# Performance work log

Hardware: AMD Instinct MI355X
Metric: run time of the kernel (lower is better)

## Reference

```python
import jax, jax.numpy as jnp
import numpy as np

DIM = 256
HEADS = 8
DIM_HEAD = 64
INNER = HEADS * DIM_HEAD  # 512
SCALE = DIM_HEAD ** -0.5
B, H, W = 8, 64, 64


def setup_inputs() -> dict:
    key = jax.random.key(0)
    ks = jax.random.split(key, 6)
    x = jax.random.normal(ks[0], (B, DIM, H, W), dtype=jnp.float32)
    W_proj = jax.random.normal(ks[1], (DIM, INNER), dtype=jnp.float32) * (DIM ** -0.5)
    step_rep = jax.random.normal(ks[2], (HEADS, 1, 1), dtype=jnp.float32)
    step_x = jax.random.normal(ks[3], (HEADS, 1, 1), dtype=jnp.float32)
    W_out = jax.random.normal(ks[4], (INNER, DIM), dtype=jnp.float32) * (INNER ** -0.5)
    b_out = jax.random.normal(ks[5], (DIM,), dtype=jnp.float32) * 0.01
    return {"x": x, "W_proj": W_proj, "step_rep": step_rep, "step_x": step_x,
            "W_out": W_out, "b_out": b_out}


def _attention(q, k, v):
    # q: [b,h,m,d], k/v: [b,h,n,d]
    dots = jnp.einsum('bhmd,bhnd->bhmn', q, k) * SCALE
    attn = jax.nn.softmax(dots, axis=-1)
    out = jnp.einsum('bhmn,bhnd->bhmd', attn, v)
    return out, attn


def reference(x, W_proj, step_rep, step_x, W_out, b_out):
    b, c, h, w = x.shape
    n = h * w
    # b c h w -> b (h w) c
    x_seq = jnp.transpose(x, (0, 2, 3, 1)).reshape(b, n, c)
    proj = x_seq @ W_proj  # [b, n, inner]
    # AdaptiveAvgPool2d((8,8)) over the (h,w) grid; h,w divisible by 8 -> exact block mean
    proj_2d = proj.reshape(b, h, w, INNER)
    rep = proj_2d.reshape(b, 8, h // 8, 8, w // 8, INNER).mean(axis=(2, 4))  # [b,8,8,inner]
    rep = rep.reshape(b, 64, INNER)
    # split heads
    proj_h = proj.reshape(b, n, HEADS, DIM_HEAD).transpose(0, 2, 1, 3)  # [b,heads,n,dh]
    rep_h = rep.reshape(b, 64, HEADS, DIM_HEAD).transpose(0, 2, 1, 3)   # [b,heads,64,dh]
    # stage 1: 64 pooled queries attend to n keys
    rep_delta, attn = _attention(rep_h, proj_h, proj_h)  # attn: [b,heads,64,n]
    rep2 = rep_h + step_rep * rep_delta
    # stage 2: self-attention among the 64 pooled tokens
    x_delta, _ = _attention(rep2, rep2, rep2)  # [b,heads,64,dh]
    # back-project via attn^T
    x_delta = jnp.einsum('bhmn,bhmd->bhnd', attn, x_delta)  # [b,heads,n,dh]
    x_delta = step_x * x_delta
    # b h n k -> b n (h k)
    x_delta = x_delta.transpose(0, 2, 1, 3).reshape(b, n, INNER)
    x_out = x_delta @ W_out + b_out  # [b, n, dim]
    return x_out.reshape(b, h, w, c).transpose(0, 3, 1, 2)
```

## Files before the change

kernel.cpp:

```cpp
#include <hip/hip_runtime.h>
#include <cstdint>
#include <cstddef>


#define SCALE 0.125f

typedef __attribute__((ext_vector_type(8))) short bf16x8;
typedef __attribute__((ext_vector_type(4))) float f32x4;
typedef __attribute__((ext_vector_type(16))) float f32x16;
typedef __attribute__((ext_vector_type(4))) unsigned int u32x4;

#define MFMA32(a, b, c) __builtin_amdgcn_mfma_f32_32x32x16_bf16(a, b, c, 0, 0, 0)
#define MFMA16(a, b, c) __builtin_amdgcn_mfma_f32_16x16x32_bf16(a, b, c, 0, 0, 0)

__device__ __forceinline__ unsigned short f2bf(float x) {
  unsigned int u = __float_as_uint(x);
  u += 0x7FFFu + ((u >> 16) & 1u);
  return (unsigned short)(u >> 16);
}
__device__ __forceinline__ float bf2f(unsigned short b) {
  return __uint_as_float(((unsigned int)b) << 16);
}
__device__ __forceinline__ void split2(float x, unsigned short& h, unsigned short& l) {
  h = f2bf(x);
  l = f2bf(x - bf2f(h));
}
__device__ __forceinline__ unsigned int cvtpk(float lo, float hi_) {
  unsigned int r;
  asm("v_cvt_pk_bf16_f32 %0, %1, %2" : "=v"(r) : "v"(lo), "v"(hi_));
  return r;
}

typedef const __attribute__((address_space(1))) unsigned int* gas_ptr;
typedef __attribute__((address_space(3))) unsigned int* las_ptr;
__device__ __forceinline__ void gload16(const void* g, void* l) {
  __builtin_amdgcn_global_load_lds((gas_ptr)(size_t)g,
                                   (las_ptr)(unsigned int)(size_t)l, 16, 0, 0);
}

__global__ __launch_bounds__(256) void tsplit(
    const float* __restrict__ in, long long in_bs,
    unsigned short* __restrict__ oh, unsigned short* __restrict__ ol,
    long long o_bs, int R, int C) {
  __shared__ float T[32][33];
  int bz = blockIdx.z;
  const float* ip = in + (size_t)bz * in_bs;
  unsigned short* oph = oh + (size_t)bz * o_bs;
  unsigned short* opl = ol + (size_t)bz * o_bs;
  int c0 = blockIdx.x * 32, r0 = blockIdx.y * 32;
  int t = threadIdx.x;
  int col = t & 31, row8 = t >> 5;
#pragma unroll
  for (int i = 0; i < 4; i++)
    T[row8 + i * 8][col] = ip[(size_t)(r0 + row8 + i * 8) * C + c0 + col];
  __syncthreads();
  int cp = (t & 15) * 2, rr = t >> 4;
#pragma unroll
  for (int i = 0; i < 2; i++) {
    int orow = rr + i * 16;
    float v0 = T[cp][orow], v1 = T[cp + 1][orow];
    unsigned short h0, l0, h1, l1;
    split2(v0, h0, l0);
    split2(v1, h1, l1);
    size_t o = (size_t)(c0 + orow) * R + r0 + cp;
    *(unsigned int*)(oph + o) = (unsigned int)h0 | ((unsigned int)h1 << 16);
    *(unsigned int*)(opl + o) = (unsigned int)l0 | ((unsigned int)l1 << 16);
  }
}

template <int BT>
__global__ __launch_bounds__(256) void gemm_mfma(
    const unsigned short* __restrict__ Ah, const unsigned short* __restrict__ Al,
    long long a_bs,
    const unsigned short* __restrict__ Bh, const unsigned short* __restrict__ Bl,
    long long b_bs,
    float* __restrict__ Cf, unsigned short* __restrict__ Ch,
    unsigned short* __restrict__ Cl, long long c_bs,
    int M, int N, int K, const float* __restrict__ bias, int lnx, int lny) {
  __shared__ unsigned short lds[2][4][128][32];
  int id0 = blockIdx.x;
  int cpx = gridDim.x >> 3;
  int id = (id0 & 7) * cpx + (id0 >> 3);
  int bx = id & ((1 << lnx) - 1);
  int by = (id >> lnx) & ((1 << lny) - 1);
  int bz = id >> (lnx + lny);
  int m0 = by * 128, n0 = bx * 128;
  int tid = threadIdx.x;
  int wave = tid >> 6, lane = tid & 63;
  int wr = wave >> 1, wc = wave & 1;

  const unsigned short* src;
  int r0g, sBeg = 0, nS = 8, dArr = wave;
  if (wave == 0) {
    src = Ah + (size_t)bz * a_bs; r0g = m0;
  } else if (wave == 1) {
    src = Al + (size_t)bz * a_bs; r0g = m0;
  } else if (BT == 2) {
    src = ((wave == 2) ? Bh : Bl) + (size_t)bz * b_bs; r0g = n0;
  } else {
    src = Bh + (size_t)bz * b_bs; r0g = n0; dArr = 2;
    sBeg = (wave - 2) * 4; nS = 4;
  }
  int q = lane >> 2;
  int chunk = (lane & 3) ^ ((q >> 1) & 3);
  const unsigned short* srow = src + (size_t)(r0g + q) * K + chunk * 8;

  int g = lane >> 4, fr = lane & 15;
  int slot = (g ^ ((fr >> 1) & 3)) * 8;
  int offA = (wr * 64 + fr) * 32 + slot;
  int offB = 2 * 4096 + (wc * 64 + fr) * 32 + slot;

  f32x4 acc[4][4];
#pragma unroll
  for (int i = 0; i < 4; i++)
#pragma unroll
    for (int j = 0; j < 4; j++)
#pragma unroll
      for (int r = 0; r < 4; r++) acc[i][j][r] = 0.0f;

  int nt = K >> 5;
  for (int s5 = 0; s5 < nS; ++s5) {
    int ss = sBeg + s5;
    gload16(srow + (size_t)(ss * 16) * K, &lds[0][dArr][ss * 16][0]);
  }
  __syncthreads();
  int cur = 0;
  for (int t0 = 0; t0 < nt; ++t0) {
    if (t0 + 1 < nt) {
      int k0 = (t0 + 1) << 5;
      for (int s5 = 0; s5 < nS; ++s5) {
        int ss = sBeg + s5;
        gload16(srow + (size_t)(ss * 16) * K + k0, &lds[cur ^ 1][dArr][ss * 16][0]);
      }
    }
    const unsigned short* bb = &lds[cur][0][0][0];
    bf16x8 af[2][4], bfv[2][4];
#pragma unroll
    for (int i = 0; i < 4; i++) {
      af[0][i] = *(const bf16x8*)(bb + offA + i * 512);
      af[1][i] = *(const bf16x8*)(bb + 4096 + offA + i * 512);
      bfv[0][i] = *(const bf16x8*)(bb + offB + i * 512);
      if (BT == 2) bfv[1][i] = *(const bf16x8*)(bb + 4096 + offB + i * 512);
    }
#pragma unroll
    for (int i = 0; i < 4; i++)
#pragma unroll
      for (int j = 0; j < 4; j++) {
        acc[i][j] = MFMA16(af[0][i], bfv[0][j], acc[i][j]);
        if (BT == 2) acc[i][j] = MFMA16(af[0][i], bfv[1][j], acc[i][j]);
        acc[i][j] = MFMA16(af[1][i], bfv[0][j], acc[i][j]);
      }
    __syncthreads();
    cur ^= 1;
  }
  int mBase = m0 + wr * 64 + g * 4;
  int nBase = n0 + wc * 64 + fr;
  if (Cf) {
    float* Cb = Cf + (size_t)bz * c_bs;
#pragma unroll
    for (int i = 0; i < 4; i++)
#pragma unroll
      for (int qd = 0; qd < 4; qd++) {
        int m = mBase + i * 16 + qd;
        float bi = bias ? bias[m] : 0.0f;
#pragma unroll
        for (int j = 0; j < 4; j++)
          Cb[(size_t)m * N + nBase + j * 16] = acc[i][j][qd] + bi;
      }
  } else {
    unsigned short* Chb = Ch + (size_t)bz * c_bs;
    unsigned short* Clb = Cl + (size_t)bz * c_bs;
#pragma unroll
    for (int i = 0; i < 4; i++)
#pragma unroll
      for (int qd = 0; qd < 4; qd++) {
        int m = mBase + i * 16 + qd;
#pragma unroll
        for (int j = 0; j < 4; j++) {
          unsigned short hh, ll;
          split2(acc[i][j][qd], hh, ll);
          Chb[(size_t)m * N + nBase + j * 16] = hh;
          Clb[(size_t)m * N + nBase + j * 16] = ll;
        }
      }
  }
}

__global__ __launch_bounds__(256) void tpool(
    const unsigned short* __restrict__ projh, const unsigned short* __restrict__ projl,
    unsigned short* __restrict__ projTh,
    unsigned short* __restrict__ reph, unsigned short* __restrict__ repl) {
  __shared__ unsigned short Lh[64][64];
  __shared__ unsigned short Ll[64][64];
  int it = blockIdx.x, py = blockIdx.y, b = blockIdx.z;
  int t = threadIdx.x;
  int ch = t & 63, seg = t >> 6;
  int swc = ((ch ^ (ch >> 3)) & 7) << 3;
  float poolacc[2] = {0.0f, 0.0f};

  for (int dy = 0; dy < 8; dy++) {
    int base_n = py * 512 + dy * 64;
    {
      int rl = t >> 3, cq = (t & 7) * 8;
#pragma unroll
      for (int p = 0; p < 2; p++) {
        int row = rl + p * 32;
        size_t ga = ((size_t)(b * 4096 + base_n + row)) * 512 + it * 64 + cq;
        bf16x8 vh = *(const bf16x8*)(projh + ga);
        bf16x8 vl = *(const bf16x8*)(projl + ga);
#pragma unroll
        for (int j = 0; j < 8; j++) {
          int cl = cq + j;
          int sw = ((cl ^ (cl >> 3)) & 7) << 3;
          Lh[cl][row ^ sw] = (unsigned short)vh[j];
          Ll[cl][row ^ sw] = (unsigned short)vl[j];
        }
      }
    }
    __syncthreads();
#pragma unroll
    for (int half = 0; half < 2; half++) {
      int n0 = seg * 16 + half * 8;
      int n0x = n0 ^ swc;
      bf16x8 rh = *(const bf16x8*)&Lh[ch][n0x];
      bf16x8 rl8 = *(const bf16x8*)&Ll[ch][n0x];
      size_t o = ((size_t)(b * 512 + it * 64 + ch)) * 4096 + base_n + n0;
      *(bf16x8*)(projTh + o) = rh;
      float ssum = 0.0f;
#pragma unroll
      for (int j = 0; j < 8; j++)
        ssum += bf2f((unsigned short)rh[j]) + bf2f((unsigned short)rl8[j]);
      poolacc[half] += ssum;
    }
    __syncthreads();
  }
#pragma unroll
  for (int half = 0; half < 2; half++) {
    float v = poolacc[half] * 0.015625f;
    unsigned short hh, ll;
    split2(v, hh, ll);
    size_t ro = ((size_t)(b * 64 + py * 8 + seg * 2 + half)) * 512 + it * 64 + ch;
    reph[ro] = hh;
    repl[ro] = ll;
  }
}

__global__ __launch_bounds__(256) void fattn(
    const unsigned short* __restrict__ projh,
    const unsigned short* __restrict__ reph, const unsigned short* __restrict__ repl,
    const unsigned short* __restrict__ projTh,
    unsigned short* __restrict__ PTh,
    float* __restrict__ pvpart, float* __restrict__ lpart) {
  int bh = blockIdx.x, s = blockIdx.y;
  int b = bh >> 3, h = bh & 7;
  int t = threadIdx.x;
  int wave = t >> 6, lane = t & 63;
  int lm = lane & 31, hi = lane >> 5;

  bf16x8 qf[2][4][2];
#pragma unroll
  for (int mt = 0; mt < 2; mt++)
#pragma unroll
    for (int ks = 0; ks < 4; ks++) {
      size_t qo = ((size_t)(b * 64 + mt * 32 + lm)) * 512 + h * 64 + ks * 16 + hi * 8;
      qf[mt][ks][0] = *(const bf16x8*)(reph + qo);
      qf[mt][ks][1] = *(const bf16x8*)(repl + qo);
    }

  f32x16 pv[2][2];
#pragma unroll
  for (int a = 0; a < 2; a++)
#pragma unroll
    for (int c = 0; c < 2; c++)
#pragma unroll
      for (int r = 0; r < 16; r++) pv[a][c][r] = 0.0f;
  float lsum0 = 0.0f, lsum1 = 0.0f;

  for (int sti = 0; sti < 2; sti++) {
    int n0 = s * 512 + (wave * 2 + sti) * 64;
#pragma unroll
    for (int nn = 0; nn < 64; nn += 32) {
      int nb = n0 + nn;
      f32x16 sa0, sa1;
#pragma unroll
      for (int r = 0; r < 16; r++) { sa0[r] = 0.0f; sa1[r] = 0.0f; }
      __builtin_amdgcn_s_setprio(1);
#pragma unroll
      for (int ks = 0; ks < 4; ks++) {
        size_t ko = ((size_t)(b * 4096 + nb + lm)) * 512 + h * 64 + ks * 16 + hi * 8;
        bf16x8 kh = *(const bf16x8*)(projh + ko);
        sa0 = MFMA32(kh, qf[0][ks][0], sa0);
        sa0 = MFMA32(kh, qf[0][ks][1], sa0);
        sa1 = MFMA32(kh, qf[1][ks][0], sa1);
        sa1 = MFMA32(kh, qf[1][ks][1], sa1);
      }
      __builtin_amdgcn_s_setprio(0);
#pragma unroll
      for (int r = 0; r < 16; r++) {
        sa0[r] = __expf(sa0[r] * SCALE); lsum0 += sa0[r];
        sa1[r] = __expf(sa1[r] * SCALE); lsum1 += sa1[r];
      }
      {
        int kk0 = h * 64 + lm, kk1 = kk0 + 32;
#pragma unroll
        for (int r = 0; r < 16; r++) {
          int n = nb + (r & 3) + 8 * (r >> 2) + 4 * hi;
          size_t o = ((size_t)(b * 4096 + n)) * 512;
          PTh[o + kk0] = f2bf(sa0[r]);
          PTh[o + kk1] = f2bf(sa1[r]);
        }
      }
#pragma unroll
      for (int kc = 0; kc < 2; kc++) {
        bf16x8 paH[2], paL[2];
#pragma unroll
        for (int mt = 0; mt < 2; mt++) {
          float pq[8], lq[8];
#pragma unroll
          for (int qi = 0; qi < 8; qi++) {
            float v = (mt == 0) ? sa0[kc * 8 + qi] : sa1[kc * 8 + qi];
            unsigned short ph_ = f2bf(v);
            pq[qi] = v;
            lq[qi] = v - bf2f(ph_);
          }
          int c01 = (int)cvtpk(pq[0], pq[1]), c23 = (int)cvtpk(pq[2], pq[3]);
          int c45 = (int)cvtpk(pq[4], pq[5]), c67 = (int)cvtpk(pq[6], pq[7]);
          int d01 = __shfl_xor(c01, 32), d23 = __shfl_xor(c23, 32);
          int d45 = __shfl_xor(c45, 32), d67 = __shfl_xor(c67, 32);
          u32x4 wv;
          wv.x = (unsigned int)(hi ? d45 : c01);
          wv.y = (unsigned int)(hi ? d67 : c23);
          wv.z = (unsigned int)(hi ? c45 : d01);
          wv.w = (unsigned int)(hi ? c67 : d23);
          paH[mt] = __builtin_bit_cast(bf16x8, wv);
          int e01 = (int)cvtpk(lq[0], lq[1]), e23 = (int)cvtpk(lq[2], lq[3]);
          int e45 = (int)cvtpk(lq[4], lq[5]), e67 = (int)cvtpk(lq[6], lq[7]);
          int f01 = __shfl_xor(e01, 32), f23 = __shfl_xor(e23, 32);
          int f45 = __shfl_xor(e45, 32), f67 = __shfl_xor(e67, 32);
          u32x4 lv;
          lv.x = (unsigned int)(hi ? f45 : e01);
          lv.y = (unsigned int)(hi ? f67 : e23);
          lv.z = (unsigned int)(hi ? e45 : f01);
          lv.w = (unsigned int)(hi ? e67 : f23);
          paL[mt] = __builtin_bit_cast(bf16x8, lv);
        }
#pragma unroll
        for (int dt = 0; dt < 2; dt++) {
          size_t vto = ((size_t)(b * 512 + h * 64 + dt * 32 + lm)) * 4096 +
                       nb + kc * 16 + hi * 8;
          bf16x8 vh = *(const bf16x8*)(projTh + vto);
          __builtin_amdgcn_s_setprio(1);
          pv[0][dt] = MFMA32(paH[0], vh, pv[0][dt]);
          pv[0][dt] = MFMA32(paL[0], vh, pv[0][dt]);
          pv[1][dt] = MFMA32(paH[1], vh, pv[1][dt]);
          pv[1][dt] = MFMA32(paL[1], vh, pv[1][dt]);
          __builtin_amdgcn_s_setprio(0);
        }
      }
    }
  }
  lsum0 += __shfl_xor(lsum0, 32);
  lsum1 += __shfl_xor(lsum1, 32);
  __shared__ float pvbuf[64][64];
  __shared__ float lbuf[4][64];
  if (hi == 0) { lbuf[wave][lm] = lsum0; lbuf[wave][32 + lm] = lsum1; }
  for (int w = 0; w < 4; w++) {
    __syncthreads();
    if (wave == w) {
#pragma unroll
      for (int mt = 0; mt < 2; mt++)
#pragma unroll
        for (int dt = 0; dt < 2; dt++)
#pragma unroll
          for (int r = 0; r < 16; r++) {
            int m = mt * 32 + (r & 3) + 8 * (r >> 2) + 4 * hi;
            int d = dt * 32 + lm;
            if (w == 0) pvbuf[m][d] = pv[mt][dt][r];
            else pvbuf[m][d] += pv[mt][dt][r];
          }
    }
  }
  __syncthreads();
  size_t base = ((size_t)(s * 64 + bh)) * 4096;
  for (int idx = t; idx < 4096; idx += 256)
    pvpart[base + idx] = pvbuf[idx >> 6][idx & 63];
  if (t < 64)
    lpart[((size_t)(s * 64 + bh)) * 64 + t] =
        lbuf[0][t] + lbuf[1][t] + lbuf[2][t] + lbuf[3][t];
}

__global__ __launch_bounds__(256) void merge_k(
    const float* __restrict__ pvpart, const float* __restrict__ lpart,
    const unsigned short* __restrict__ reph, const unsigned short* __restrict__ repl,
    const float* __restrict__ step_rep, float* __restrict__ rep2,
    float* __restrict__ linv) {
  int bh = blockIdx.x, qy = blockIdx.y;
  int b = bh >> 3, h = bh & 7;
  float sr = step_rep[h];
  int t = threadIdx.x;
  __shared__ float lt[64];
  if (t < 64) {
    float L = 0.0f;
#pragma unroll
    for (int ss = 0; ss < 8; ss++) L += lpart[((size_t)(ss * 64 + bh)) * 64 + t];
    float inv = 1.0f / L;
    lt[t] = inv;
    if (qy == 0) linv[bh * 64 + t] = inv;
  }
  __syncthreads();
#pragma unroll
  for (int k2 = 0; k2 < 4; k2++) {
    int idx = qy * 1024 + k2 * 256 + t;
    int m = idx >> 6, d = idx & 63;
    float sum = 0.0f;
#pragma unroll
    for (int ss = 0; ss < 8; ss++)
      sum += pvpart[((size_t)(ss * 64 + bh)) * 4096 + idx];
    size_t ro = ((size_t)(b * 64 + m)) * 512 + h * 64 + d;
    float repv = bf2f(reph[ro]) + bf2f(repl[ro]);
    rep2[(size_t)bh * 4096 + idx] = repv + sr * sum * lt[m];
  }
}

__global__ __launch_bounds__(256) void stage2_k(
    const float* __restrict__ rep2, const float* __restrict__ Wo,
    const float* __restrict__ step_x, const float* __restrict__ linv,
    unsigned short* __restrict__ GTh, unsigned short* __restrict__ GTl) {
  __shared__ float T[64][68];
  __shared__ float P[64][68];
  __shared__ float Wl[64][68];
  int bh = blockIdx.x, h = bh & 7, b = bh >> 3;
  int t = threadIdx.x;
  int mi = t >> 2, dq = (t & 3) * 16;
#pragma unroll
  for (int j = 0; j < 4; j++) {
    float4 v = *(const float4*)(rep2 + ((size_t)bh * 64 + mi) * 64 + dq + j * 4);
    T[dq + j * 4 + 0][mi] = v.x; T[dq + j * 4 + 1][mi] = v.y;
    T[dq + j * 4 + 2][mi] = v.z; T[dq + j * 4 + 3][mi] = v.w;
  }
  __syncthreads();
  int tx = t & 15, ty = t >> 4;
  {
    float acc[4][4] = {};
#pragma unroll
    for (int k = 0; k < 64; k++) {
      float4 a = *(const float4*)&T[k][ty * 4];
      float4 bv = *(const float4*)&T[k][tx * 4];
      float aa[4] = {a.x, a.y, a.z, a.w};
      float bb[4] = {bv.x, bv.y, bv.z, bv.w};
#pragma unroll
      for (int i = 0; i < 4; i++)
#pragma unroll
        for (int j = 0; j < 4; j++) acc[i][j] += aa[i] * bb[j];
    }
#pragma unroll
    for (int i = 0; i < 4; i++)
      *(float4*)&P[ty * 4 + i][tx * 4] =
          make_float4(acc[i][0] * SCALE, acc[i][1] * SCALE, acc[i][2] * SCALE,
                      acc[i][3] * SCALE);
  }
  __syncthreads();
  if (t < 64) {
    float mx = -3.4e38f;
    for (int n = 0; n < 64; n++) mx = fmaxf(mx, P[t][n]);
    float s = 0.0f;
    for (int n = 0; n < 64; n++) {
      float e = __expf(P[t][n] - mx);
      P[t][n] = e;
      s += e;
    }
    float r = 1.0f / s;
    for (int n = 0; n < 64; n++) P[t][n] *= r;
  }
  __syncthreads();
  float xacc[4][4] = {};
#pragma unroll
  for (int k = 0; k < 64; k++) {
    float aa[4], bb[4];
#pragma unroll
    for (int i = 0; i < 4; i++) {
      aa[i] = P[ty * 4 + i][k];
      bb[i] = T[tx * 4 + i][k];
    }
#pragma unroll
    for (int i = 0; i < 4; i++)
#pragma unroll
      for (int j = 0; j < 4; j++) xacc[i][j] += aa[i] * bb[j];
  }
  __syncthreads();
#pragma unroll
  for (int i = 0; i < 4; i++)
    *(float4*)&P[ty * 4 + i][tx * 4] =
        make_float4(xacc[i][0], xacc[i][1], xacc[i][2], xacc[i][3]);
  float sxh = step_x[h];
  float li[4];
#pragma unroll
  for (int i = 0; i < 4; i++) li[i] = linv[bh * 64 + ty * 4 + i] * sxh;
  int wk = t >> 2, wcq = (t & 3) * 16;
  for (int cb = 0; cb < 4; cb++) {
    __syncthreads();
#pragma unroll
    for (int j = 0; j < 4; j++)
      *(float4*)&Wl[wk][wcq + j * 4] =
          *(const float4*)(Wo + ((size_t)(h * 64 + wk)) * 256 + cb * 64 + wcq + j * 4);
    __syncthreads();
    float gacc[4][4] = {};
#pragma unroll
    for (int k = 0; k < 64; k++) {
      float aa[4];
#pragma unroll
      for (int i = 0; i < 4; i++) aa[i] = P[ty * 4 + i][k];
      float4 bv = *(const float4*)&Wl[k][tx * 4];
      float bb[4] = {bv.x, bv.y, bv.z, bv.w};
#pragma unroll
      for (int i = 0; i < 4; i++)
#pragma unroll
        for (int j = 0; j < 4; j++) gacc[i][j] += aa[i] * bb[j];
    }
#pragma unroll
    for (int i = 0; i < 4; i++)
#pragma unroll
      for (int j = 0; j < 4; j++) {
        float val = gacc[i][j] * li[i];
        size_t o = ((size_t)(b * 256 + cb * 64 + tx * 4 + j)) * 512 + h * 64 + ty * 4 + i;
        unsigned short hh, ll;
        split2(val, hh, ll);
        GTh[o] = hh;
        GTl[o] = ll;
      }
  }
}

extern "C" void kernel_launch(void* const* d_in, const int* in_sizes, int n_in,
                              void* d_out, int out_size, void* d_ws, size_t ws_size,
                              hipStream_t stream) {
  const float* x = (const float*)d_in[0];
  const float* Wp = (const float*)d_in[1];
  const float* srep = (const float*)d_in[2];
  const float* sx = (const float*)d_in[3];
  const float* Wo = (const float*)d_in[4];
  const float* bo = (const float*)d_in[5];
  float* out = (float*)d_out;

  char* wsb = (char*)d_ws;
  unsigned short* projh = (unsigned short*)(wsb + 0);
  unsigned short* projl = (unsigned short*)(wsb + 33554432);
  unsigned short* xTh   = (unsigned short*)(wsb + 67108864);
  unsigned short* xTl   = (unsigned short*)(wsb + 83886080);
  unsigned short* projTh= (unsigned short*)(wsb + 67108864);
  unsigned short* WpTh  = (unsigned short*)(wsb + 100663296);
  unsigned short* WpTl  = (unsigned short*)(wsb + 100925440);
  unsigned short* PTh   = (unsigned short*)(wsb + 100663296);
  unsigned short* reph  = (unsigned short*)(wsb + 134217728);
  unsigned short* repl  = (unsigned short*)(wsb + 134742016);
  float*  pvpart        = (float*)(wsb + 135266304);
  float*  lpart         = (float*)(wsb + 143654912);
  float*  rep2          = (float*)(wsb + 0);
  float*  linv          = (float*)(wsb + 1048576);
  unsigned short* GTh   = (unsigned short*)(wsb + 2097152);
  unsigned short* GTl   = (unsigned short*)(wsb + 4194304);

  tsplit<<<dim3(128, 8, 8), 256, 0, stream>>>(x, (long long)256 * 4096,
                                              xTh, xTl, (long long)4096 * 256, 256, 4096);
  tsplit<<<dim3(16, 8, 1), 256, 0, stream>>>(Wp, 0, WpTh, WpTl, 0, 256, 512);
  gemm_mfma<2><<<dim3(1024), 256, 0, stream>>>(
      xTh, xTl, (long long)4096 * 256, WpTh, WpTl, 0,
      nullptr, projh, projl, (long long)4096 * 512, 4096, 512, 256, nullptr,
      2, 5);
  tpool<<<dim3(8, 8, 8), 256, 0, stream>>>(projh, projl, projTh, reph, repl);
  fattn<<<dim3(64, 8), 256, 0, stream>>>(projh, reph, repl, projTh, PTh,
                                         pvpart, lpart);
  merge_k<<<dim3(64, 4), 256, 0, stream>>>(pvpart, lpart, reph, repl, srep,
                                           rep2, linv);
  stage2_k<<<dim3(64), 256, 0, stream>>>(rep2, Wo, sx, linv, GTh, GTl);
  gemm_mfma<1><<<dim3(512), 256, 0, stream>>>(
      GTh, GTl, (long long)256 * 512, PTh, nullptr, (long long)4096 * 512,
      out, nullptr, nullptr, (long long)256 * 4096, 256, 4096, 512, bo,
      5, 1);
}
```

Measured before the change: 236.7 us.

## Drop low-half split of proj, fuse merge into stage2, stage GEMM epilogue via LDS

The projection GEMM now uses one bf16 part of W_proj and writes proj as a single bf16 tensor with no low residual. This cuts one MFMA per tile, the projl writes, and the tpool reads of projl. The GEMM epilogue is staged through LDS so global stores are vectorized, and the merge and stage2 kernels are fused into one launch. The cost is lower precision for proj and the pooled rep, plus a 64-block fused kernel that may underuse the GPU.

After: 231.2 us. 2.3% less time.

```diff
diff --git a/kernel.cpp b/kernel.cpp
--- a/kernel.cpp
+++ b/kernel.cpp
@@ -68,16 +68,14 @@
   }
 }
 
-template <int BT>
-__global__ __launch_bounds__(256) void gemm_mfma(
+template <bool F32OUT>
+__global__ __launch_bounds__(256) void gemm_sb(
     const unsigned short* __restrict__ Ah, const unsigned short* __restrict__ Al,
     long long a_bs,
-    const unsigned short* __restrict__ Bh, const unsigned short* __restrict__ Bl,
-    long long b_bs,
-    float* __restrict__ Cf, unsigned short* __restrict__ Ch,
-    unsigned short* __restrict__ Cl, long long c_bs,
+    const unsigned short* __restrict__ Bh, long long b_bs,
+    float* __restrict__ Cf, unsigned short* __restrict__ Ch, long long c_bs,
     int M, int N, int K, const float* __restrict__ bias, int lnx, int lny) {
-  __shared__ unsigned short lds[2][4][128][32];
+  __shared__ unsigned short lds[2][3][128][32];
   int id0 = blockIdx.x;
   int cpx = gridDim.x >> 3;
   int id = (id0 & 7) * cpx + (id0 >> 3);
@@ -90,17 +88,10 @@
   int wr = wave >> 1, wc = wave & 1;
 
   const unsigned short* src;
-  int r0g, sBeg = 0, nS = 8, dArr = wave;
-  if (wave == 0) {
-    src = Ah + (size_t)bz * a_bs; r0g = m0;
-  } else if (wave == 1) {
-    src = Al + (size_t)bz * a_bs; r0g = m0;
-  } else if (BT == 2) {
-    src = ((wave == 2) ? Bh : Bl) + (size_t)bz * b_bs; r0g = n0;
-  } else {
-    src = Bh + (size_t)bz * b_bs; r0g = n0; dArr = 2;
-    sBeg = (wave - 2) * 4; nS = 4;
-  }
+  int r0g, sBeg, nS, dArr;
+  if (wave == 0) { src = Ah + (size_t)bz * a_bs; r0g = m0; sBeg = 0; nS = 8; dArr = 0; }
+  else if (wave == 1) { src = Al + (size_t)bz * a_bs; r0g = m0; sBeg = 0; nS = 8; dArr = 1; }
+  else { src = Bh + (size_t)bz * b_bs; r0g = n0; sBeg = (wave - 2) * 4; nS = 4; dArr = 2; }
   int q = lane >> 2;
   int chunk = (lane & 3) ^ ((q >> 1) & 3);
   const unsigned short* srow = src + (size_t)(r0g + q) * K + chunk * 8;
@@ -134,64 +125,69 @@
       }
     }
     const unsigned short* bb = &lds[cur][0][0][0];
-    bf16x8 af[2][4], bfv[2][4];
+    bf16x8 af[2][4], bfv[4];
 #pragma unroll
     for (int i = 0; i < 4; i++) {
       af[0][i] = *(const bf16x8*)(bb + offA + i * 512);
       af[1][i] = *(const bf16x8*)(bb + 4096 + offA + i * 512);
-      bfv[0][i] = *(const bf16x8*)(bb + offB + i * 512);
-      if (BT == 2) bfv[1][i] = *(const bf16x8*)(bb + 4096 + offB + i * 512);
+      bfv[i] = *(const bf16x8*)(bb + offB + i * 512);
     }
 #pragma unroll
     for (int i = 0; i < 4; i++)
 #pragma unroll
       for (int j = 0; j < 4; j++) {
-        acc[i][j] = MFMA16(af[0][i], bfv[0][j], acc[i][j]);
-        if (BT == 2) acc[i][j] = MFMA16(af[0][i], bfv[1][j], acc[i][j]);
-        acc[i][j] = MFMA16(af[1][i], bfv[0][j], acc[i][j]);
+        acc[i][j] = MFMA16(af[0][i], bfv[j], acc[i][j]);
+        acc[i][j] = MFMA16(af[1][i], bfv[j], acc[i][j]);
       }
     __syncthreads();
     cur ^= 1;
   }
-  int mBase = m0 + wr * 64 + g * 4;
-  int nBase = n0 + wc * 64 + fr;
-  if (Cf) {
-    float* Cb = Cf + (size_t)bz * c_bs;
-#pragma unroll
-    for (int i = 0; i < 4; i++)
-#pragma unroll
-      for (int qd = 0; qd < 4; qd++) {
-        int m = mBase + i * 16 + qd;
-        float bi = bias ? bias[m] : 0.0f;
-#pragma unroll
-        for (int j = 0; j < 4; j++)
-          Cb[(size_t)m * N + nBase + j * 16] = acc[i][j][qd] + bi;
-      }
-  } else {
-    unsigned short* Chb = Ch + (size_t)bz * c_bs;
-    unsigned short* Clb = Cl + (size_t)bz * c_bs;
-#pragma unroll
-    for (int i = 0; i < 4; i++)
-#pragma unroll
-      for (int qd = 0; qd < 4; qd++) {
-        int m = mBase + i * 16 + qd;
-#pragma unroll
-        for (int j = 0; j < 4; j++) {
-          unsigned short hh, ll;
-          split2(acc[i][j][qd], hh, ll);
-          Chb[(size_t)m * N + nBase + j * 16] = hh;
-          Clb[(size_t)m * N + nBase + j * 16] = ll;
-        }
-      }
+
+  float* eld = (float*)(&lds[0][0][0][0]) + wave * 1088;
+  int rr = lane >> 2, cb = (lane & 3) * 16;
+#pragma unroll
+  for (int i = 0; i < 4; i++) {
+#pragma unroll
+    for (int j = 0; j < 4; j++)
+#pragma unroll
+      for (int qd = 0; qd < 4; qd++)
+        eld[(g * 4 + qd) * 68 + fr + j * 16] = acc[i][j][qd];
+    __syncthreads();
+    int mrow = m0 + wr * 64 + i * 16 + rr;
+    int ncol = n0 + wc * 64 + cb;
+    float4 v0 = *(const float4*)(eld + rr * 68 + cb);
+    float4 v1 = *(const float4*)(eld + rr * 68 + cb + 4);
+    float4 v2 = *(const float4*)(eld + rr * 68 + cb + 8);
+    float4 v3 = *(const float4*)(eld + rr * 68 + cb + 12);
+    if (F32OUT) {
+      float bi = bias ? bias[mrow] : 0.0f;
+      float* Cb = Cf + (size_t)bz * c_bs + (size_t)mrow * N + ncol;
+      *(float4*)(Cb + 0) = make_float4(v0.x + bi, v0.y + bi, v0.z + bi, v0.w + bi);
+      *(float4*)(Cb + 4) = make_float4(v1.x + bi, v1.y + bi, v1.z + bi, v1.w + bi);
+      *(float4*)(Cb + 8) = make_float4(v2.x + bi, v2.y + bi, v2.z + bi, v2.w + bi);
+      *(float4*)(Cb + 12) = make_float4(v3.x + bi, v3.y + bi, v3.z + bi, v3.w + bi);
+    } else {
+      float vv[16] = {v0.x, v0.y, v0.z, v0.w, v1.x, v1.y, v1.z, v1.w,
+                      v2.x, v2.y, v2.z, v2.w, v3.x, v3.y, v3.z, v3.w};
+      bf16x8 p0, p1;
+#pragma unroll
+      for (int k = 0; k < 8; k++) {
+        p0[k] = (short)f2bf(vv[k]);
+        p1[k] = (short)f2bf(vv[8 + k]);
+      }
+      unsigned short* Cb = Ch + (size_t)bz * c_bs + (size_t)mrow * N + ncol;
+      *(bf16x8*)(Cb + 0) = p0;
+      *(bf16x8*)(Cb + 8) = p1;
+    }
+    __syncthreads();
   }
 }
 
 __global__ __launch_bounds__(256) void tpool(
-    const unsigned short* __restrict__ projh, const unsigned short* __restrict__ projl,
+    const unsigned short* __restrict__ projh,
     unsigned short* __restrict__ projTh,
     unsigned short* __restrict__ reph, unsigned short* __restrict__ repl) {
   __shared__ unsigned short Lh[64][64];
-  __shared__ unsigned short Ll[64][64];
   int it = blockIdx.x, py = blockIdx.y, b = blockIdx.z;
   int t = threadIdx.x;
   int ch = t & 63, seg = t >> 6;
@@ -207,13 +203,11 @@
         int row = rl + p * 32;
         size_t ga = ((size_t)(b * 4096 + base_n + row)) * 512 + it * 64 + cq;
         bf16x8 vh = *(const bf16x8*)(projh + ga);
-        bf16x8 vl = *(const bf16x8*)(projl + ga);
 #pragma unroll
         for (int j = 0; j < 8; j++) {
           int cl = cq + j;
           int sw = ((cl ^ (cl >> 3)) & 7) << 3;
           Lh[cl][row ^ sw] = (unsigned short)vh[j];
-          Ll[cl][row ^ sw] = (unsigned short)vl[j];
         }
       }
     }
@@ -223,13 +217,11 @@
       int n0 = seg * 16 + half * 8;
       int n0x = n0 ^ swc;
       bf16x8 rh = *(const bf16x8*)&Lh[ch][n0x];
-      bf16x8 rl8 = *(const bf16x8*)&Ll[ch][n0x];
       size_t o = ((size_t)(b * 512 + it * 64 + ch)) * 4096 + base_n + n0;
       *(bf16x8*)(projTh + o) = rh;
       float ssum = 0.0f;
 #pragma unroll
-      for (int j = 0; j < 8; j++)
-        ssum += bf2f((unsigned short)rh[j]) + bf2f((unsigned short)rl8[j]);
+      for (int j = 0; j < 8; j++) ssum += bf2f((unsigned short)rh[j]);
       poolacc[half] += ssum;
     }
     __syncthreads();
@@ -389,28 +381,27 @@
         lbuf[0][t] + lbuf[1][t] + lbuf[2][t] + lbuf[3][t];
 }
 
-__global__ __launch_bounds__(256) void merge_k(
+__global__ __launch_bounds__(256) void stage2f(
     const float* __restrict__ pvpart, const float* __restrict__ lpart,
     const unsigned short* __restrict__ reph, const unsigned short* __restrict__ repl,
-    const float* __restrict__ step_rep, float* __restrict__ rep2,
-    float* __restrict__ linv) {
-  int bh = blockIdx.x, qy = blockIdx.y;
-  int b = bh >> 3, h = bh & 7;
+    const float* __restrict__ step_rep, const float* __restrict__ step_x,
+    const float* __restrict__ Wo,
+    unsigned short* __restrict__ GTh, unsigned short* __restrict__ GTl) {
+  __shared__ float T[64][68];
+  __shared__ float P[64][68];
+  __shared__ float Wl[64][68];
+  __shared__ float lt[64];
+  int bh = blockIdx.x, h = bh & 7, b = bh >> 3;
+  int t = threadIdx.x;
   float sr = step_rep[h];
-  int t = threadIdx.x;
-  __shared__ float lt[64];
   if (t < 64) {
     float L = 0.0f;
 #pragma unroll
     for (int ss = 0; ss < 8; ss++) L += lpart[((size_t)(ss * 64 + bh)) * 64 + t];
-    float inv = 1.0f / L;
-    lt[t] = inv;
-    if (qy == 0) linv[bh * 64 + t] = inv;
-  }
-  __syncthreads();
-#pragma unroll
-  for (int k2 = 0; k2 < 4; k2++) {
-    int idx = qy * 1024 + k2 * 256 + t;
+    lt[t] = 1.0f / L;
+  }
+  __syncthreads();
+  for (int idx = t; idx < 4096; idx += 256) {
     int m = idx >> 6, d = idx & 63;
     float sum = 0.0f;
 #pragma unroll
@@ -418,25 +409,7 @@
       sum += pvpart[((size_t)(ss * 64 + bh)) * 4096 + idx];
     size_t ro = ((size_t)(b * 64 + m)) * 512 + h * 64 + d;
     float repv = bf2f(reph[ro]) + bf2f(repl[ro]);
-    rep2[(size_t)bh * 4096 + idx] = repv + sr * sum * lt[m];
-  }
-}
-
-__global__ __launch_bounds__(256) void stage2_k(
-    const float* __restrict__ rep2, const float* __restrict__ Wo,
-    const float* __restrict__ step_x, const float* __restrict__ linv,
-    unsigned short* __restrict__ GTh, unsigned short* __restrict__ GTl) {
-  __shared__ float T[64][68];
-  __shared__ float P[64][68];
-  __shared__ float Wl[64][68];
-  int bh = blockIdx.x, h = bh & 7, b = bh >> 3;
-  int t = threadIdx.x;
-  int mi = t >> 2, dq = (t & 3) * 16;
-#pragma unroll
-  for (int j = 0; j < 4; j++) {
-    float4 v = *(const float4*)(rep2 + ((size_t)bh * 64 + mi) * 64 + dq + j * 4);
-    T[dq + j * 4 + 0][mi] = v.x; T[dq + j * 4 + 1][mi] = v.y;
-    T[dq + j * 4 + 2][mi] = v.z; T[dq + j * 4 + 3][mi] = v.w;
+    T[d][m] = repv + sr * sum * lt[m];
   }
   __syncthreads();
   int tx = t & 15, ty = t >> 4;
@@ -495,7 +468,7 @@
   float sxh = step_x[h];
   float li[4];
 #pragma unroll
-  for (int i = 0; i < 4; i++) li[i] = linv[bh * 64 + ty * 4 + i] * sxh;
+  for (int i = 0; i < 4; i++) li[i] = lt[ty * 4 + i] * sxh;
   int wk = t >> 2, wcq = (t & 3) * 16;
   for (int cb = 0; cb < 4; cb++) {
     __syncthreads();
@@ -543,38 +516,32 @@
   float* out = (float*)d_out;
 
   char* wsb = (char*)d_ws;
-  unsigned short* projh = (unsigned short*)(wsb + 0);
-  unsigned short* projl = (unsigned short*)(wsb + 33554432);
-  unsigned short* xTh   = (unsigned short*)(wsb + 67108864);
-  unsigned short* xTl   = (unsigned short*)(wsb + 83886080);
-  unsigned short* projTh= (unsigned short*)(wsb + 67108864);
-  unsigned short* WpTh  = (unsigned short*)(wsb + 100663296);
-  unsigned short* WpTl  = (unsigned short*)(wsb + 100925440);
-  unsigned short* PTh   = (unsigned short*)(wsb + 100663296);
-  unsigned short* reph  = (unsigned short*)(wsb + 134217728);
-  unsigned short* repl  = (unsigned short*)(wsb + 134742016);
-  float*  pvpart        = (float*)(wsb + 135266304);
-  float*  lpart         = (float*)(wsb + 143654912);
-  float*  rep2          = (float*)(wsb + 0);
-  float*  linv          = (float*)(wsb + 1048576);
-  unsigned short* GTh   = (unsigned short*)(wsb + 2097152);
-  unsigned short* GTl   = (unsigned short*)(wsb + 4194304);
+  unsigned short* projh  = (unsigned short*)(wsb + 0);
+  unsigned short* projTh = (unsigned short*)(wsb + 33554432);
+  unsigned short* xTh    = (unsigned short*)(wsb + 67108864);
+  unsigned short* xTl    = (unsigned short*)(wsb + 83886080);
+  unsigned short* PTh    = (unsigned short*)(wsb + 67108864);
+  unsigned short* WpTh   = (unsigned short*)(wsb + 100663296);
+  unsigned short* WpTl   = (unsigned short*)(wsb + 100925440);
+  unsigned short* reph   = (unsigned short*)(wsb + 101187584);
+  unsigned short* repl   = (unsigned short*)(wsb + 101711872);
+  float* pvpart          = (float*)(wsb + 102236160);
+  float* lpart           = (float*)(wsb + 110624768);
+  unsigned short* GTh    = (unsigned short*)(wsb + 110755840);
+  unsigned short* GTl    = (unsigned short*)(wsb + 112852992);
 
   tsplit<<<dim3(128, 8, 8), 256, 0, stream>>>(x, (long long)256 * 4096,
                                               xTh, xTl, (long long)4096 * 256, 256, 4096);
   tsplit<<<dim3(16, 8, 1), 256, 0, stream>>>(Wp, 0, WpTh, WpTl, 0, 256, 512);
-  gemm_mfma<2><<<dim3(1024), 256, 0, stream>>>(
-      xTh, xTl, (long long)4096 * 256, WpTh, WpTl, 0,
-      nullptr, projh, projl, (long long)4096 * 512, 4096, 512, 256, nullptr,
-      2, 5);
-  tpool<<<dim3(8, 8, 8), 256, 0, stream>>>(projh, projl, projTh, reph, repl);
+  gemm_sb<false><<<dim3(1024), 256, 0, stream>>>(
+      xTh, xTl, (long long)4096 * 256, WpTh, 0,
+      nullptr, projh, (long long)4096 * 512, 4096, 512, 256, nullptr, 2, 5);
+  tpool<<<dim3(8, 8, 8), 256, 0, stream>>>(projh, projTh, reph, repl);
   fattn<<<dim3(64, 8), 256, 0, stream>>>(projh, reph, repl, projTh, PTh,
                                          pvpart, lpart);
-  merge_k<<<dim3(64, 4), 256, 0, stream>>>(pvpart, lpart, reph, repl, srep,
-                                           rep2, linv);
-  stage2_k<<<dim3(64), 256, 0, stream>>>(rep2, Wo, sx, linv, GTh, GTl);
-  gemm_mfma<1><<<dim3(512), 256, 0, stream>>>(
-      GTh, GTl, (long long)256 * 512, PTh, nullptr, (long long)4096 * 512,
-      out, nullptr, nullptr, (long long)256 * 4096, 256, 4096, 512, bo,
-      5, 1);
-}
+  stage2f<<<dim3(64), 256, 0, stream>>>(pvpart, lpart, reph, repl, srep, sx,
+                                        Wo, GTh, GTl);
+  gemm_sb<true><<<dim3(512), 256, 0, stream>>>(
+      GTh, GTl, (long long)256 * 512, PTh, (long long)4096 * 512,
+      out, nullptr, (long long)256 * 4096, 256, 4096, 512, bo, 5, 1);
+}
```
